# Optimization experiments

Measured on AMD Instinct MI355X. Metric: run time of the kernel, lower is better.

The kernel has to match this reference:

```python
import jax, jax.numpy as jnp
import numpy as np

B, S, I, H, O = 64, 1024, 256, 512, 256


def setup_inputs() -> dict:
    key = jax.random.key(0)
    ks = jax.random.split(key, 13)
    s = 0.02
    return {
        "x": jax.random.normal(ks[0], (B, S, I), dtype=jnp.float32),
        "U_w": jax.random.normal(ks[1], (H, I), dtype=jnp.float32) * s,
        "U_b": jax.random.normal(ks[2], (H,), dtype=jnp.float32) * s,
        "W_w": jax.random.normal(ks[3], (H, H), dtype=jnp.float32) * s,
        "W_b": jax.random.normal(ks[4], (H,), dtype=jnp.float32) * s,
        "V_w": jax.random.normal(ks[5], (H, H), dtype=jnp.float32) * s,
        "V_b": jax.random.normal(ks[6], (H,), dtype=jnp.float32) * s,
        "fc1_w": jax.random.normal(ks[7], (H, H), dtype=jnp.float32) * s,
        "fc1_b": jax.random.normal(ks[8], (H,), dtype=jnp.float32) * s,
        "fc2_w": jax.random.normal(ks[9], (H, H), dtype=jnp.float32) * s,
        "fc2_b": jax.random.normal(ks[10], (H,), dtype=jnp.float32) * s,
        "fc3_w": jax.random.normal(ks[11], (O, H), dtype=jnp.float32) * s,
        "fc3_b": jax.random.normal(ks[12], (O,), dtype=jnp.float32) * s,
    }


def reference(x, U_w, U_b, W_w, W_b, V_w, V_b, fc1_w, fc1_b, fc2_w, fc2_b, fc3_w, fc3_b):
    # x: [B, S, I] (batch_first). Time-major for the recurrence: [S, B, I]
    xt = jnp.swapaxes(x, 0, 1)
    # Input projection U(x_t) is time-independent: precompute once. [S, B, H]
    xu = jnp.einsum('sbi,hi->sbh', xt, U_w) + U_b

    def step(h_prev, xu_t):
        # a_t = U x_t + W h_{t-1}; h_t = tanh(a_t); o_t = V h_t
        h_t = jnp.tanh(xu_t + h_prev @ W_w.T + W_b)
        o_t = h_t @ V_w.T + V_b
        return h_t, o_t

    h0 = jnp.zeros((x.shape[0], W_w.shape[0]), dtype=x.dtype)
    _, out = jax.lax.scan(step, h0, xu)  # out: [S, B, H]

    # MLP head (dropout layers are identity in eval mode)
    out = out @ fc1_w.T + fc1_b
    out = out @ fc2_w.T + fc2_b
    out = out @ fc3_w.T + fc3_b  # [S, B, O]
    return jnp.swapaxes(out, 0, 1)  # [B, S, O]
```

## Files before the change

### kernel.cpp

```cpp
#include <hip/hip_runtime.h>
#include <hip/hip_bf16.h>

typedef __attribute__((ext_vector_type(8))) short short8;
typedef __attribute__((ext_vector_type(4))) float f32x4;

#define B_ 64
#define S_ 1024
#define I_ 256
#define H_ 512
#define O_ 256
#define M_ (B_ * S_)

__device__ __forceinline__ ushort bf16_rne(float f) {
  unsigned u = __float_as_uint(f);
  return (ushort)((u + 0x7FFFu + ((u >> 16) & 1u)) >> 16);
}
__device__ __forceinline__ float bf16_f(ushort s) {
  return __uint_as_float(((unsigned)s) << 16);
}
__device__ __forceinline__ void gll16(const void* g, void* l) {
  __builtin_amdgcn_global_load_lds((const __attribute__((address_space(1))) void*)g,
                                   (__attribute__((address_space(3))) void*)l, 16, 0, 0);
}
__device__ __forceinline__ float tanh_fast(float a) {
  a = fminf(fmaxf(a, -9.0f), 9.0f);
#if __has_builtin(__builtin_amdgcn_exp2f)
  float t = __builtin_amdgcn_exp2f(a * 2.8853900817779268f);
#else
  float t = exp2f(a * 2.8853900817779268f);
#endif
#if __has_builtin(__builtin_amdgcn_rcpf)
  return (t - 1.0f) * __builtin_amdgcn_rcpf(t + 1.0f);
#else
  return (t - 1.0f) / (t + 1.0f);
#endif
}

__global__ void cvt_kern(const float* __restrict__ in, ushort* __restrict__ out, long n) {
  long i = ((long)blockIdx.x * blockDim.x + threadIdx.x) * 4;
  const long stride = (long)gridDim.x * blockDim.x * 4;
  for (; i < n; i += stride) {
    const float4 v = *(const float4*)(in + i);
    ushort4 o;
    o.x = bf16_rne(v.x); o.y = bf16_rne(v.y); o.z = bf16_rne(v.z); o.w = bf16_rne(v.w);
    *(ushort4*)(out + i) = o;
  }
}

__global__ void biascomb_kern(const float* __restrict__ a, const float* __restrict__ b,
                              float* __restrict__ o) {
  int i = threadIdx.x;
  o[i] = a[i] + b[i];
}

__global__ __launch_bounds__(256) void f32gemm_kern(
    const float* __restrict__ A, const float* __restrict__ Bm,
    float* __restrict__ C, int M, int N, int K)
{
  __shared__ float As[16][16];
  __shared__ float Bs[16][17];
  const int tx = threadIdx.x & 15, ty = threadIdx.x >> 4;
  const int row = blockIdx.y * 16 + ty, col = blockIdx.x * 16 + tx;
  float acc = 0.0f;
  for (int k0 = 0; k0 < K; k0 += 16) {
    As[ty][tx] = A[(size_t)row * K + k0 + tx];
    Bs[ty][tx] = Bm[(size_t)(k0 + ty) * N + col];
    __syncthreads();
    #pragma unroll
    for (int kk = 0; kk < 16; ++kk) acc += As[ty][kk] * Bs[kk][tx];
    __syncthreads();
  }
  C[(size_t)row * N + col] = acc;
}

__global__ void matvec_kern(const float* __restrict__ Mw, const float* __restrict__ x,
                            const float* __restrict__ b, float* __restrict__ y, int R, int C) {
  const int i = blockIdx.x * blockDim.x + threadIdx.x;
  if (i >= R) return;
  float acc = b[i];
  for (int k = 0; k < C; ++k) acc += Mw[(size_t)i * C + k] * x[k];
  y[i] = acc;
}

template<bool OUT_F32>
__global__ __launch_bounds__(256) void gemm_kern(
    const ushort* __restrict__ A, const ushort* __restrict__ Wt,
    const float* __restrict__ bias, void* __restrict__ out,
    int M, int N, int K)
{
  __shared__ char smem[16384];
  const int tid = threadIdx.x;
  const int lane = tid & 63, wave = tid >> 6;
  const int wm = wave >> 1, wn = wave & 1;
  const int nt = N >> 7;
  const int bm = blockIdx.x / nt, bn = blockIdx.x % nt;
  const long m0 = (long)bm * 128, n0 = (long)bn * 128;

  f32x4 acc[4][4] = {};
  const int KT = K >> 5;
  for (int kt = 0; kt < KT; ++kt) {
    #pragma unroll
    for (int i = 0; i < 4; ++i) {
      const int c = wave * 4 + i;
      const int isB = c >> 3;
      const int cc = c & 7;
      const int kgrp = cc >> 1, rhalf = cc & 1;
      const int row = rhalf * 64 + lane;
      const ushort* src = (isB ? Wt + (n0 + row) * (long)K : A + (m0 + row) * (long)K)
                          + (long)kt * 32 + kgrp * 8;
      gll16(src, smem + isB * 8192 + kgrp * 2048 + rhalf * 1024);
    }
    __syncthreads();
    const char* Ab = smem + (lane >> 4) * 2048;
    const char* Bb = smem + 8192 + (lane >> 4) * 2048;
    short8 af[4], bf[4];
    #pragma unroll
    for (int i = 0; i < 4; ++i) {
      af[i] = *(const short8*)(Ab + (wm * 64 + i * 16 + (lane & 15)) * 16);
      bf[i] = *(const short8*)(Bb + (wn * 64 + i * 16 + (lane & 15)) * 16);
    }
    #pragma unroll
    for (int mi = 0; mi < 4; ++mi)
      #pragma unroll
      for (int ni = 0; ni < 4; ++ni)
        acc[mi][ni] = __builtin_amdgcn_mfma_f32_16x16x32_bf16(af[mi], bf[ni], acc[mi][ni], 0, 0, 0);
    __syncthreads();
  }
  #pragma unroll
  for (int ni = 0; ni < 4; ++ni) {
    const long n = n0 + wn * 64 + ni * 16 + (lane & 15);
    const float bv = bias[n];
    #pragma unroll
    for (int mi = 0; mi < 4; ++mi) {
      const long mrow = m0 + wm * 64 + mi * 16 + (lane >> 4) * 4;
      #pragma unroll
      for (int r = 0; r < 4; ++r) {
        const float v = acc[mi][ni][r] + bv;
        if (OUT_F32) ((float*)out)[(mrow + r) * (long)N + n] = v;
        else         ((ushort*)out)[(mrow + r) * (long)N + n] = bf16_rne(v);
      }
    }
  }
}

__global__ __launch_bounds__(512, 2) void rec_kern(
    const ushort* __restrict__ XU,
    const ushort* __restrict__ Wb,
    ushort* __restrict__ Hst)
{
  extern __shared__ char smem[];
  const int tid = threadIdx.x;
  const int lane = tid & 63;
  const int wave = tid >> 6;
  const int b = lane & 15;
  const int hi = lane >> 4;
  const int bg = blockIdx.x << 4;
  const int swz = (b & 7) << 4;

  #pragma unroll
  for (int i = 0; i < 16; ++i) {
    const int ch = wave * 16 + i;
    const int s = 12 + (ch >> 5);
    const int mt = ch & 31;
    const ushort* src = Wb + (size_t)(mt * 16 + b) * H_ + s * 32 + hi * 8;
    gll16(src, smem + 32768 + (size_t)(s - 12) * 32768 + mt * 1024);
  }
  {
    f32x4 zz = 0.0f;
    *(f32x4*)(smem + tid * 64) = zz;
    *(f32x4*)(smem + tid * 64 + 16) = zz;
    *(f32x4*)(smem + tid * 64 + 32) = zz;
    *(f32x4*)(smem + tid * 64 + 48) = zz;
  }
  short8 wreg[4][12];
  #pragma unroll
  for (int mt = 0; mt < 4; ++mt) {
    const int mtg = wave * 4 + mt;
    const ushort* wrow = Wb + (size_t)(mtg * 16 + b) * H_ + hi * 8;
    #pragma unroll
    for (int s = 0; s < 12; ++s)
      wreg[mt][s] = *(const short8*)(wrow + s * 32);
  }
  #pragma unroll
  for (int mt = 0; mt < 4; ++mt)
    #pragma unroll
    for (int s = 0; s < 12; ++s)
      asm volatile("" : "+v"(wreg[mt][s]));
  __syncthreads();

  const ushort* xup = XU + (size_t)(bg + b) * S_ * H_ + wave * 64 + hi * 4;
  ushort* hgp = Hst + (size_t)(bg + b) * S_ * H_ + wave * 64 + hi * 4;
  const int hoff = b * 1024;
  const int woff = (wave * 128 + hi * 8);

  for (int t = 0; t < S_; ++t) {
    uint2 xu[4];
    #pragma unroll
    for (int mt = 0; mt < 4; ++mt)
      xu[mt] = *(const uint2*)(xup + mt * 16);
    xup += H_;

    const char* hb = smem + (t & 1) * 16384 + hoff;
    f32x4 acc[4] = {};
    #pragma unroll
    for (int s = 0; s < 16; ++s) {
      const short8 bfrag = *(const short8*)(hb + ((s * 64 + hi * 16) ^ swz));
      #pragma unroll
      for (int mt = 0; mt < 4; ++mt) {
        short8 w;
        if (s < 12) w = wreg[mt][s];
        else w = *(const short8*)(smem + 32768 + (s - 12) * 32768 + (wave * 4 + mt) * 1024 + lane * 16);
        acc[mt] = __builtin_amdgcn_mfma_f32_16x16x32_bf16(w, bfrag, acc[mt], 0, 0, 0);
      }
    }
    char* hw = smem + ((t + 1) & 1) * 16384 + hoff;
    #pragma unroll
    for (int mt = 0; mt < 4; ++mt) {
      ushort4 hp;
      #pragma unroll
      for (int r = 0; r < 4; ++r) {
        const ushort xb = ((const ushort*)&xu[mt])[r];
        const float a = acc[mt][r] + bf16_f(xb);
        ((ushort*)&hp)[r] = bf16_rne(tanh_fast(a));
      }
      *(uint2*)(hw + ((woff + mt * 32) ^ swz)) = *(uint2*)&hp;
      *(uint2*)(hgp + mt * 16) = *(uint2*)&hp;
    }
    hgp += H_;
    __syncthreads();
  }
}

extern "C" void kernel_launch(void* const* d_in, const int* in_sizes, int n_in,
                              void* d_out, int out_size, void* d_ws, size_t ws_size,
                              hipStream_t stream) {
  const float* x     = (const float*)d_in[0];
  const float* U_w   = (const float*)d_in[1];
  const float* U_b   = (const float*)d_in[2];
  const float* W_w   = (const float*)d_in[3];
  const float* W_b   = (const float*)d_in[4];
  const float* V_w   = (const float*)d_in[5];
  const float* V_b   = (const float*)d_in[6];
  const float* fc1_w = (const float*)d_in[7];
  const float* fc1_b = (const float*)d_in[8];
  const float* fc2_w = (const float*)d_in[9];
  const float* fc2_b = (const float*)d_in[10];
  const float* fc3_w = (const float*)d_in[11];
  const float* fc3_b = (const float*)d_in[12];

  char* ws = (char*)d_ws;
  ushort* Hst  = (ushort*)ws;
  ushort* xb16 = (ushort*)(ws + 67108864);
  char*   wb   = ws + 134217728;
  ushort* U_wb = (ushort*)wb;
  ushort* W_wb = U_wb + 131072;
  ushort* Wcb  = W_wb + 262144;
  float*  C1   = (float*)(Wcb + 131072);
  float*  C2   = C1 + 262144;
  float*  Wcf  = C2 + 262144;
  float*  cbias = Wcf + 131072;
  float*  t1   = cbias + 512;
  float*  t2   = t1 + 512;
  float*  bc   = t2 + 512;
  ushort* bufA = (ushort*)d_out;

  cvt_kern<<<2048, 256, 0, stream>>>(x, xb16, (long)M_ * I_);
  cvt_kern<<<128, 256, 0, stream>>>(U_w, U_wb, (long)H_ * I_);
  cvt_kern<<<256, 256, 0, stream>>>(W_w, W_wb, (long)H_ * H_);
  biascomb_kern<<<1, 512, 0, stream>>>(U_b, W_b, cbias);

  f32gemm_kern<<<dim3(32, 32), 256, 0, stream>>>(fc1_w, V_w, C1, H_, H_, H_);
  f32gemm_kern<<<dim3(32, 32), 256, 0, stream>>>(fc2_w, C1, C2, H_, H_, H_);
  f32gemm_kern<<<dim3(32, 16), 256, 0, stream>>>(fc3_w, C2, Wcf, O_, H_, H_);
  matvec_kern<<<2, 256, 0, stream>>>(fc1_w, V_b, fc1_b, t1, H_, H_);
  matvec_kern<<<2, 256, 0, stream>>>(fc2_w, t1, fc2_b, t2, H_, H_);
  matvec_kern<<<1, 256, 0, stream>>>(fc3_w, t2, fc3_b, bc, O_, H_);
  cvt_kern<<<128, 256, 0, stream>>>(Wcf, Wcb, (long)O_ * H_);

  gemm_kern<false><<<dim3(512 * 4), 256, 0, stream>>>(xb16, U_wb, cbias, bufA, M_, H_, I_);

  hipFuncSetAttribute((const void*)rec_kern, hipFuncAttributeMaxDynamicSharedMemorySize, 163840);
  rec_kern<<<dim3(4), dim3(512), 163840, stream>>>(bufA, W_wb, Hst);

  gemm_kern<true><<<dim3(512 * 2), 256, 0, stream>>>(Hst, Wcb, bc, d_out, M_, O_, H_);

  (void)in_sizes; (void)n_in; (void)out_size; (void)ws_size;
}
```

Measured before the change: 2.818 ms.

## Split recurrence across 8 workgroups of 8 batches and prescale tanh inputs

The recurrent kernel now runs 8 workgroups of 256 threads, each handling 8 batch rows instead of 16, with each wave covering 8 M-tiles and keeping more W in registers. The 2/ln2 factor of tanh is folded into the bf16 weights and bias up front, and packed bf16 conversion replaces manual rounding. The aim is more compute units working on the serial recurrence with fewer instructions per step. The cost is that half the MFMA lanes carry padding, since only 8 of 16 batch columns hold real data, and register pressure rises from doubling the per-wave weight tiles.

Result: slower. 4.935 ms (+75.2%).

```diff
diff --git a/kernel.cpp b/kernel.cpp
--- a/kernel.cpp
+++ b/kernel.cpp
@@ -10,6 +10,9 @@
 #define H_ 512
 #define O_ 256
 #define M_ (B_ * S_)
+#define NB 8
+#define NWG 8
+#define SC 2.8853900817779268f
 
 __device__ __forceinline__ ushort bf16_rne(float f) {
   unsigned u = __float_as_uint(f);
@@ -18,17 +21,18 @@
 __device__ __forceinline__ float bf16_f(ushort s) {
   return __uint_as_float(((unsigned)s) << 16);
 }
+__device__ __forceinline__ unsigned cvt_pk_bf16(float lo, float hi) {
+  unsigned r;
+  asm("v_cvt_pk_bf16_f32 %0, %1, %2" : "=v"(r) : "v"(lo), "v"(hi));
+  return r;
+}
 __device__ __forceinline__ void gll16(const void* g, void* l) {
   __builtin_amdgcn_global_load_lds((const __attribute__((address_space(1))) void*)g,
                                    (__attribute__((address_space(3))) void*)l, 16, 0, 0);
 }
-__device__ __forceinline__ float tanh_fast(float a) {
-  a = fminf(fmaxf(a, -9.0f), 9.0f);
-#if __has_builtin(__builtin_amdgcn_exp2f)
-  float t = __builtin_amdgcn_exp2f(a * 2.8853900817779268f);
-#else
-  float t = exp2f(a * 2.8853900817779268f);
-#endif
+__device__ __forceinline__ float tanh_pre(float a) {
+  a = fminf(fmaxf(a, -26.0f), 26.0f);
+  float t = exp2f(a);
 #if __has_builtin(__builtin_amdgcn_rcpf)
   return (t - 1.0f) * __builtin_amdgcn_rcpf(t + 1.0f);
 #else
@@ -36,13 +40,15 @@
 #endif
 }
 
-__global__ void cvt_kern(const float* __restrict__ in, ushort* __restrict__ out, long n) {
+__global__ void cvt_kern(const float* __restrict__ in, ushort* __restrict__ out, long n,
+                         float scale) {
   long i = ((long)blockIdx.x * blockDim.x + threadIdx.x) * 4;
   const long stride = (long)gridDim.x * blockDim.x * 4;
   for (; i < n; i += stride) {
     const float4 v = *(const float4*)(in + i);
     ushort4 o;
-    o.x = bf16_rne(v.x); o.y = bf16_rne(v.y); o.z = bf16_rne(v.z); o.w = bf16_rne(v.w);
+    o.x = bf16_rne(v.x * scale); o.y = bf16_rne(v.y * scale);
+    o.z = bf16_rne(v.z * scale); o.w = bf16_rne(v.w * scale);
     *(ushort4*)(out + i) = o;
   }
 }
@@ -50,7 +56,7 @@
 __global__ void biascomb_kern(const float* __restrict__ a, const float* __restrict__ b,
                               float* __restrict__ o) {
   int i = threadIdx.x;
-  o[i] = a[i] + b[i];
+  o[i] = (a[i] + b[i]) * SC;
 }
 
 __global__ __launch_bounds__(256) void f32gemm_kern(
@@ -143,7 +149,7 @@
   }
 }
 
-__global__ __launch_bounds__(512, 2) void rec_kern(
+__global__ __launch_bounds__(256, 1) void rec_kern(
     const ushort* __restrict__ XU,
     const ushort* __restrict__ Wb,
     ushort* __restrict__ Hst)
@@ -154,16 +160,14 @@
   const int wave = tid >> 6;
   const int b = lane & 15;
   const int hi = lane >> 4;
-  const int bg = blockIdx.x << 4;
-  const int swz = (b & 7) << 4;
-
-  #pragma unroll
-  for (int i = 0; i < 16; ++i) {
-    const int ch = wave * 16 + i;
-    const int s = 12 + (ch >> 5);
-    const int mt = ch & 31;
-    const ushort* src = Wb + (size_t)(mt * 16 + b) * H_ + s * 32 + hi * 8;
-    gll16(src, smem + 32768 + (size_t)(s - 12) * 32768 + mt * 1024);
+  const int c = b & 7;
+  const int bg = blockIdx.x * NB;
+  const int swz = c << 4;
+
+  #pragma unroll
+  for (int i = 0; i < 32; ++i) {
+    const ushort* src = Wb + (size_t)(i * 16 + b) * H_ + (12 + wave) * 32 + hi * 8;
+    gll16(src, smem + 16384 + (size_t)wave * 32768 + i * 1024);
   }
   {
     f32x4 zz = 0.0f;
@@ -172,59 +176,61 @@
     *(f32x4*)(smem + tid * 64 + 32) = zz;
     *(f32x4*)(smem + tid * 64 + 48) = zz;
   }
-  short8 wreg[4][12];
-  #pragma unroll
-  for (int mt = 0; mt < 4; ++mt) {
-    const int mtg = wave * 4 + mt;
-    const ushort* wrow = Wb + (size_t)(mtg * 16 + b) * H_ + hi * 8;
+  short8 wreg[8][12];
+  #pragma unroll
+  for (int mt = 0; mt < 8; ++mt) {
+    const ushort* wrow = Wb + (size_t)((wave * 8 + mt) * 16 + b) * H_ + hi * 8;
     #pragma unroll
     for (int s = 0; s < 12; ++s)
       wreg[mt][s] = *(const short8*)(wrow + s * 32);
   }
   #pragma unroll
-  for (int mt = 0; mt < 4; ++mt)
+  for (int mt = 0; mt < 8; ++mt)
     #pragma unroll
     for (int s = 0; s < 12; ++s)
       asm volatile("" : "+v"(wreg[mt][s]));
   __syncthreads();
 
-  const ushort* xup = XU + (size_t)(bg + b) * S_ * H_ + wave * 64 + hi * 4;
-  ushort* hgp = Hst + (size_t)(bg + b) * S_ * H_ + wave * 64 + hi * 4;
-  const int hoff = b * 1024;
-  const int woff = (wave * 128 + hi * 8);
+  const ushort* xup = XU + (size_t)(bg + c) * S_ * H_ + wave * 128 + hi * 4;
+  ushort* hgp = Hst + (size_t)(bg + b) * S_ * H_ + wave * 128 + hi * 4;
 
   for (int t = 0; t < S_; ++t) {
-    uint2 xu[4];
-    #pragma unroll
-    for (int mt = 0; mt < 4; ++mt)
+    uint2 xu[8];
+    #pragma unroll
+    for (int mt = 0; mt < 8; ++mt)
       xu[mt] = *(const uint2*)(xup + mt * 16);
     xup += H_;
 
-    const char* hb = smem + (t & 1) * 16384 + hoff;
-    f32x4 acc[4] = {};
+    const char* hb = smem + (t & 1) * 8192 + c * 1024;
+    f32x4 acc[8] = {};
     #pragma unroll
     for (int s = 0; s < 16; ++s) {
       const short8 bfrag = *(const short8*)(hb + ((s * 64 + hi * 16) ^ swz));
       #pragma unroll
-      for (int mt = 0; mt < 4; ++mt) {
+      for (int mt = 0; mt < 8; ++mt) {
         short8 w;
         if (s < 12) w = wreg[mt][s];
-        else w = *(const short8*)(smem + 32768 + (s - 12) * 32768 + (wave * 4 + mt) * 1024 + lane * 16);
+        else w = *(const short8*)(smem + 16384 + (s - 12) * 32768 + (wave * 8 + mt) * 1024 + lane * 16);
         acc[mt] = __builtin_amdgcn_mfma_f32_16x16x32_bf16(w, bfrag, acc[mt], 0, 0, 0);
       }
     }
-    char* hw = smem + ((t + 1) & 1) * 16384 + hoff;
-    #pragma unroll
-    for (int mt = 0; mt < 4; ++mt) {
-      ushort4 hp;
-      #pragma unroll
-      for (int r = 0; r < 4; ++r) {
-        const ushort xb = ((const ushort*)&xu[mt])[r];
-        const float a = acc[mt][r] + bf16_f(xb);
-        ((ushort*)&hp)[r] = bf16_rne(tanh_fast(a));
+    uint2 hv[8];
+    #pragma unroll
+    for (int mt = 0; mt < 8; ++mt) {
+      float h0 = tanh_pre(acc[mt][0] + bf16_f((ushort)(xu[mt].x & 0xFFFFu)));
+      float h1 = tanh_pre(acc[mt][1] + bf16_f((ushort)(xu[mt].x >> 16)));
+      float h2 = tanh_pre(acc[mt][2] + bf16_f((ushort)(xu[mt].y & 0xFFFFu)));
+      float h3 = tanh_pre(acc[mt][3] + bf16_f((ushort)(xu[mt].y >> 16)));
+      hv[mt].x = cvt_pk_bf16(h0, h1);
+      hv[mt].y = cvt_pk_bf16(h2, h3);
+    }
+    char* hw = smem + ((t + 1) & 1) * 8192 + c * 1024;
+    if (b < 8) {
+      #pragma unroll
+      for (int mt = 0; mt < 8; ++mt) {
+        *(uint2*)(hw + ((wave * 256 + mt * 32 + hi * 8) ^ swz)) = hv[mt];
+        *(uint2*)(hgp + mt * 16) = hv[mt];
       }
-      *(uint2*)(hw + ((woff + mt * 32) ^ swz)) = *(uint2*)&hp;
-      *(uint2*)(hgp + mt * 16) = *(uint2*)&hp;
     }
     hgp += H_;
     __syncthreads();
@@ -264,9 +270,9 @@
   float*  bc   = t2 + 512;
   ushort* bufA = (ushort*)d_out;
 
-  cvt_kern<<<2048, 256, 0, stream>>>(x, xb16, (long)M_ * I_);
-  cvt_kern<<<128, 256, 0, stream>>>(U_w, U_wb, (long)H_ * I_);
-  cvt_kern<<<256, 256, 0, stream>>>(W_w, W_wb, (long)H_ * H_);
+  cvt_kern<<<2048, 256, 0, stream>>>(x, xb16, (long)M_ * I_, 1.0f);
+  cvt_kern<<<128, 256, 0, stream>>>(U_w, U_wb, (long)H_ * I_, SC);
+  cvt_kern<<<256, 256, 0, stream>>>(W_w, W_wb, (long)H_ * H_, SC);
   biascomb_kern<<<1, 512, 0, stream>>>(U_b, W_b, cbias);
 
   f32gemm_kern<<<dim3(32, 32), 256, 0, stream>>>(fc1_w, V_w, C1, H_, H_, H_);
@@ -275,12 +281,12 @@
   matvec_kern<<<2, 256, 0, stream>>>(fc1_w, V_b, fc1_b, t1, H_, H_);
   matvec_kern<<<2, 256, 0, stream>>>(fc2_w, t1, fc2_b, t2, H_, H_);
   matvec_kern<<<1, 256, 0, stream>>>(fc3_w, t2, fc3_b, bc, O_, H_);
-  cvt_kern<<<128, 256, 0, stream>>>(Wcf, Wcb, (long)O_ * H_);
+  cvt_kern<<<128, 256, 0, stream>>>(Wcf, Wcb, (long)O_ * H_, 1.0f);
 
   gemm_kern<false><<<dim3(512 * 4), 256, 0, stream>>>(xb16, U_wb, cbias, bufA, M_, H_, I_);
 
-  hipFuncSetAttribute((const void*)rec_kern, hipFuncAttributeMaxDynamicSharedMemorySize, 163840);
-  rec_kern<<<dim3(4), dim3(512), 163840, stream>>>(bufA, W_wb, Hst);
+  hipFuncSetAttribute((const void*)rec_kern, hipFuncAttributeMaxDynamicSharedMemorySize, 147456);
+  rec_kern<<<dim3(NWG), dim3(256), 147456, stream>>>(bufA, W_wb, Hst);
 
   gemm_kern<true><<<dim3(512 * 2), 256, 0, stream>>>(Hst, Wcb, bc, d_out, M_, O_, H_);
 
```
